# Optimization experiments

Hardware: AMD Instinct MI355X
Metric: run time of the kernel (lower is better)

## Reference

```python
import jax, jax.numpy as jnp
import numpy as np

N, B, C, IC = 4096, 4, 64, 32  # seq len, batch, in_channels, inter_channels
BN_EPS = 1e-5


def setup_inputs() -> dict:
    key = jax.random.key(0)
    ks = jax.random.split(key, 12)
    s = 0.05
    return {
        "x_thisBranch": jax.random.normal(ks[0], (N, B, C), jnp.float32),
        "x_otherBranch": jax.random.normal(ks[1], (N, B, C), jnp.float32),
        "g_w": jax.random.normal(ks[2], (IC, C), jnp.float32) * s,
        "g_b": jax.random.normal(ks[3], (IC,), jnp.float32) * s,
        "theta_w": jax.random.normal(ks[4], (IC, C), jnp.float32) * s,
        "theta_b": jax.random.normal(ks[5], (IC,), jnp.float32) * s,
        "phi_w": jax.random.normal(ks[6], (IC, C), jnp.float32) * s,
        "phi_b": jax.random.normal(ks[7], (IC,), jnp.float32) * s,
        "wz_w": jax.random.normal(ks[8], (C, IC), jnp.float32) * s,
        "wz_b": jax.random.normal(ks[9], (C,), jnp.float32) * s,
        "bn_gamma": jax.random.normal(ks[10], (C,), jnp.float32) * s + 1.0,
        "bn_beta": jax.random.normal(ks[11], (C,), jnp.float32) * s,
    }


def reference(x_thisBranch, x_otherBranch, g_w, g_b, theta_w, theta_b,
              phi_w, phi_b, wz_w, wz_b, bn_gamma, bn_beta):
    # [N,B,C] -> [B,C,N] as in torch permute(1,2,0)
    xt = jnp.transpose(x_thisBranch, (1, 2, 0))   # (B,C,N)
    xo = jnp.transpose(x_otherBranch, (1, 2, 0))  # (B,C,N)

    # 1x1 conv1d == per-position linear over channels
    g_x = jnp.einsum('ic,bcn->bni', g_w, xt) + g_b            # (B,N,IC)
    theta_x = jnp.einsum('ic,bcn->bin', theta_w, xt) + theta_b[:, None]  # (B,IC,N)
    phi_x = jnp.einsum('ic,bcn->bni', phi_w, xo) + phi_b      # (B,N,IC)

    # f = phi_x @ theta_x : rows indexed by other-branch positions
    f = jnp.einsum('bni,bim->bnm', phi_x, theta_x)            # (B,N,N)
    a = jax.nn.softmax(f, axis=-1)                            # embedded mode

    y = jnp.einsum('bnm,bmi->bni', a, g_x)                    # (B,N,IC)
    y = jnp.transpose(y, (0, 2, 1))                           # (B,IC,N)

    # W_z: 1x1 conv + BatchNorm1d (training-mode batch stats)
    wy = jnp.einsum('ci,bin->bcn', wz_w, y) + wz_b[:, None]   # (B,C,N)
    mean = wy.mean(axis=(0, 2), keepdims=True)
    var = wy.var(axis=(0, 2), keepdims=True)
    wy = (wy - mean) / jnp.sqrt(var + BN_EPS) * bn_gamma[:, None] + bn_beta[:, None]

    return wy + xt
```

## Files before the change

### kernel.cpp

```cpp
#include <hip/hip_runtime.h>
#include <hip/hip_bf16.h>
#include <math.h>

typedef unsigned short ushort_t;
typedef __attribute__((ext_vector_type(8))) short short8;
typedef __attribute__((ext_vector_type(4))) float float4v;

#define NN 4096
#define BB 4
#define CC 64
#define ICH 32

#define OFF_QB 0
#define OFF_KB 262144
#define OFF_VT 524288
#define OFF_OP 786432

static __device__ __forceinline__ ushort_t f2b(float f) {
  union { float f; unsigned u; } v;
  v.f = f;
  return (ushort_t)((v.u + 0x8000u) >> 16);
}
static __device__ __forceinline__ unsigned pack2(float x, float y) {
  return (unsigned)f2b(x) | ((unsigned)f2b(y) << 16);
}
static __device__ __forceinline__ short8 cvt8lds(const float* p) {
  short8 r;
#pragma unroll
  for (int j = 0; j < 8; j++) r[j] = (short)f2b(p[j]);
  return r;
}

__global__ __launch_bounds__(256) void proj_kernel(
    const float* __restrict__ xt, const float* __restrict__ xo,
    const float* __restrict__ gw, const float* __restrict__ gb,
    const float* __restrict__ tw, const float* __restrict__ tb,
    const float* __restrict__ pw, const float* __restrict__ pb,
    ushort_t* __restrict__ Qb, ushort_t* __restrict__ Kb,
    ushort_t* __restrict__ Vt) {
  __shared__ float xls[64 * 68];
  __shared__ float wls[ICH * 68];
  __shared__ float bls[ICH];
  __shared__ ushort_t ol[2304];

  int t = threadIdx.x;
  int wv = t >> 6, lane = t & 63, l15 = lane & 15, quad = lane >> 4;
  int b = blockIdx.y, z = blockIdx.z;
  int n0 = blockIdx.x * 64;

  const float* xsrc = (z == 1) ? xo : xt;
  const float* W = (z == 0) ? tw : (z == 1) ? pw : gw;
  const float* Bv = (z == 0) ? tb : (z == 1) ? pb : gb;

#pragma unroll
  for (int it = 0; it < 4; it++) {
    int lin = it * 256 + t;
    int row = lin >> 4, seg = lin & 15;
    float4 v = *(const float4*)(xsrc + ((size_t)(n0 + row) * BB + b) * CC + seg * 4);
    *(float4*)(xls + row * 68 + seg * 4) = v;
  }
#pragma unroll
  for (int it = 0; it < 2; it++) {
    int lin = it * 256 + t;
    int row = lin >> 4, seg = lin & 15;
    float4 v = *(const float4*)(W + (size_t)row * CC + seg * 4);
    *(float4*)(wls + row * 68 + seg * 4) = v;
  }
  if (t < ICH) bls[t] = Bv[t];
  __syncthreads();

  const float* xr = xls + (wv * 16 + l15) * 68;
  short8 a0 = cvt8lds(xr + quad * 8);
  short8 a1 = cvt8lds(xr + 32 + quad * 8);

#pragma unroll
  for (int h = 0; h < 2; h++) {
    int i = h * 16 + l15;
    short8 b0 = cvt8lds(wls + i * 68 + quad * 8);
    short8 b1 = cvt8lds(wls + i * 68 + 32 + quad * 8);
    float bias = bls[i];
    float4v acc = {bias, bias, bias, bias};
    acc = __builtin_amdgcn_mfma_f32_16x16x32_bf16(a0, b0, acc, 0, 0, 0);
    acc = __builtin_amdgcn_mfma_f32_16x16x32_bf16(a1, b1, acc, 0, 0, 0);
    if (z < 2) {
#pragma unroll
      for (int r = 0; r < 4; r++)
        ol[(wv * 16 + quad * 4 + r) * 36 + i] = f2b(acc[r]);
    } else {
#pragma unroll
      for (int r = 0; r < 4; r++)
        ol[i * 68 + wv * 16 + quad * 4 + r] = f2b(acc[r]);
    }
  }
  __syncthreads();

  if (z < 2) {
    ushort_t* dst = (z == 0) ? Kb : Qb;
    int row = t >> 2, seg = t & 3;
    short8 v;
#pragma unroll
    for (int k = 0; k < 8; k++) v[k] = (short)ol[row * 36 + seg * 8 + k];
    *(short8*)(dst + ((size_t)b * NN + n0 + row) * ICH + seg * 8) = v;
  } else {
    int i = t & 31, seg = t >> 5;
    short8 v;
#pragma unroll
    for (int k = 0; k < 8; k++) v[k] = (short)ol[i * 68 + seg * 8 + k];
    *(short8*)(Vt + (size_t)(b * ICH + i) * NN + n0 + seg * 8) = v;
  }
}

__global__ __launch_bounds__(256) void attn_kernel(
    const ushort_t* __restrict__ Qb, const ushort_t* __restrict__ Kb,
    const ushort_t* __restrict__ Vt, float* __restrict__ OP,
    float* __restrict__ LS, int splits) {
  int t = threadIdx.x;
  int wv = t >> 6, lane = t & 63, l15 = lane & 15, quad = lane >> 4;
  int s = blockIdx.y, b = blockIdx.z;
  int q0 = blockIdx.x * 256 + wv * 64;
  int kspan = NN / splits;

  short8 qf[4];
#pragma unroll
  for (int f = 0; f < 4; f++)
    qf[f] = *(const short8*)(Qb + ((size_t)b * NN + q0 + f * 16 + l15) * ICH +
                             quad * 8);

  float4v o[4][2];
#pragma unroll
  for (int f = 0; f < 4; f++) {
    o[f][0] = (float4v){0.f, 0.f, 0.f, 0.f};
    o[f][1] = (float4v){0.f, 0.f, 0.f, 0.f};
  }
  float lsp[4] = {0.f, 0.f, 0.f, 0.f};

  const ushort_t* Kbb = Kb + (size_t)b * NN * ICH;
  const ushort_t* Vtb = Vt + (size_t)b * ICH * NN;
  int mbeg = s * kspan, mend = mbeg + kspan;

  const bool lowq = (quad < 2);
  const bool evenq = ((quad & 1) == 0);

  for (int m0 = mbeg; m0 < mend; m0 += 32) {
    const ushort_t* kp = Kbb + (size_t)(m0 + l15) * ICH + quad * 8;
    short8 kf0 = *(const short8*)(kp);
    short8 kf1 = *(const short8*)(kp + 16 * ICH);
    const ushort_t* vp = Vtb + (size_t)l15 * NN + m0 + quad * 8;
    short8 vf0 = *(const short8*)(vp);
    short8 vf1 = *(const short8*)(vp + 16 * NN);

#pragma unroll
    for (int f = 0; f < 4; f++) {
      float4v z = {0.f, 0.f, 0.f, 0.f};
      float4v st0 = __builtin_amdgcn_mfma_f32_16x16x32_bf16(kf0, qf[f], z, 0, 0, 0);
      float4v st1 = __builtin_amdgcn_mfma_f32_16x16x32_bf16(kf1, qf[f], z, 0, 0, 0);

      float p0[4], p1[4];
#pragma unroll
      for (int r = 0; r < 4; r++) {
        p0[r] = __expf(fminf(st0[r], 60.f));
        p1[r] = __expf(fminf(st1[r], 60.f));
        lsp[f] += p0[r] + p1[r];
      }
      unsigned d0 = pack2(p0[0], p0[1]);
      unsigned d1 = pack2(p0[2], p0[3]);
      unsigned d2 = pack2(p1[0], p1[1]);
      unsigned d3 = pack2(p1[2], p1[3]);
      unsigned e0 = lowq ? d2 : d0, e1 = lowq ? d3 : d1;
      unsigned k0 = lowq ? d0 : d2, k1 = lowq ? d1 : d3;
      unsigned r0 = (unsigned)__shfl_xor((int)e0, 32, 64);
      unsigned r1 = (unsigned)__shfl_xor((int)e1, 32, 64);
      unsigned a0 = lowq ? k0 : r0;
      unsigned a1 = lowq ? k1 : r1;
      unsigned a2 = lowq ? r0 : k0;
      unsigned a3 = lowq ? r1 : k1;
      unsigned f0 = evenq ? a2 : a0, f1 = evenq ? a3 : a1;
      unsigned g0 = evenq ? a0 : a2, g1 = evenq ? a1 : a3;
      unsigned s0w = (unsigned)__shfl_xor((int)f0, 16, 64);
      unsigned s1w = (unsigned)__shfl_xor((int)f1, 16, 64);
      unsigned w0 = evenq ? g0 : s0w;
      unsigned w1 = evenq ? g1 : s1w;
      unsigned w2 = evenq ? s0w : g0;
      unsigned w3 = evenq ? s1w : g1;

      union { unsigned u[4]; short8 s8; } pu;
      pu.u[0] = w0; pu.u[1] = w1; pu.u[2] = w2; pu.u[3] = w3;
      short8 pf = pu.s8;

      o[f][0] = __builtin_amdgcn_mfma_f32_16x16x32_bf16(pf, vf0, o[f][0], 0, 0, 0);
      o[f][1] = __builtin_amdgcn_mfma_f32_16x16x32_bf16(pf, vf1, o[f][1], 0, 0, 0);
    }
  }

  size_t base = (size_t)(b * splits + s) * NN;
#pragma unroll
  for (int f = 0; f < 4; f++) {
    float v = lsp[f];
    v += __shfl_xor(v, 16, 64);
    v += __shfl_xor(v, 32, 64);
    if (quad == 0) LS[base + q0 + f * 16 + l15] = v;
#pragma unroll
    for (int r = 0; r < 4; r++) {
      int q = q0 + f * 16 + quad * 4 + r;
      float* op = OP + (base + q) * ICH;
      op[l15] = o[f][0][r];
      op[16 + l15] = o[f][1][r];
    }
  }
}

__global__ __launch_bounds__(256) void wz_kernel(
    const float* __restrict__ OP, const float* __restrict__ LS,
    const float* __restrict__ wz_w, const float* __restrict__ wz_b,
    float* __restrict__ WY, float* __restrict__ SP, int splits) {
  __shared__ float yl[64 * 36];
  __shared__ float lsum[64];
  __shared__ float red1[256], red2[256];

  int b = blockIdx.y, n0 = blockIdx.x * 64, t = threadIdx.x;
  int blkid = b * 64 + blockIdx.x;

  if (t < 64) {
    float ssum = 0.f;
    for (int sp = 0; sp < splits; sp++)
      ssum += LS[(size_t)(b * splits + sp) * NN + n0 + t];
    lsum[t] = ssum;
  }
  __syncthreads();
#pragma unroll
  for (int it = 0; it < 8; it++) {
    int lin = it * 256 + t;
    int i = lin & 31, dn = lin >> 5;
    float sacc = 0.f;
    for (int sp = 0; sp < splits; sp++)
      sacc += OP[((size_t)(b * splits + sp) * NN + n0 + dn) * ICH + i];
    yl[dn * 36 + i] = sacc / lsum[dn];
  }
  __syncthreads();

  int c = t >> 2, sub = t & 3;
  float4 w4[8];
#pragma unroll
  for (int j = 0; j < 8; j++) w4[j] = ((const float4*)(wz_w + c * ICH))[j];
  float bc = wz_b[c];
  float s1 = 0.f, s2 = 0.f;
#pragma unroll
  for (int d = 0; d < 16; d++) {
    int dn = sub * 16 + d;
    const float4* y4 = (const float4*)(yl + dn * 36);
    float acc = bc;
#pragma unroll
    for (int j = 0; j < 8; j++) {
      float4 y = y4[j];
      acc += w4[j].x * y.x + w4[j].y * y.y + w4[j].z * y.z + w4[j].w * y.w;
    }
    WY[((size_t)(b * CC + c)) * NN + n0 + dn] = acc;
    s1 += acc;
    s2 += acc * acc;
  }
  red1[t] = s1;
  red2[t] = s2;
  __syncthreads();
  if (t < 64) {
    float a1 = red1[t * 4] + red1[t * 4 + 1] + red1[t * 4 + 2] + red1[t * 4 + 3];
    float a2 = red2[t * 4] + red2[t * 4 + 1] + red2[t * 4 + 2] + red2[t * 4 + 3];
    SP[(size_t)blkid * 64 + t] = a1;
    SP[16384 + (size_t)blkid * 64 + t] = a2;
  }
}

__global__ __launch_bounds__(256) void stats_kernel(
    const float* __restrict__ SP, const float* __restrict__ gamma,
    const float* __restrict__ beta, float* __restrict__ AB) {
  __shared__ double r1[256], r2[256];
  int c = blockIdx.x, t = threadIdx.x;
  r1[t] = (double)SP[(size_t)t * 64 + c];
  r2[t] = (double)SP[16384 + (size_t)t * 64 + c];
  __syncthreads();
  for (int off = 128; off > 0; off >>= 1) {
    if (t < off) {
      r1[t] += r1[t + off];
      r2[t] += r2[t + off];
    }
    __syncthreads();
  }
  if (t == 0) {
    double inv = 1.0 / (double)(BB * NN);
    double mean = r1[0] * inv;
    double var = r2[0] * inv - mean * mean;
    if (var < 0.0) var = 0.0;
    double rstd = 1.0 / sqrt(var + 1e-5);
    float A = gamma[c] * (float)rstd;
    AB[c] = A;
    AB[64 + c] = beta[c] - (float)mean * A;
  }
}

__global__ __launch_bounds__(256) void norm_kernel(
    const float* __restrict__ WY, const float* __restrict__ AB,
    const float* __restrict__ xthis, float* __restrict__ out) {
  __shared__ float xl[64 * 65];
  __shared__ float abr[128];
  int b = blockIdx.y, n0 = blockIdx.x * 64, t = threadIdx.x;
  if (t < 128) abr[t] = AB[t];
#pragma unroll
  for (int it = 0; it < 16; it++) {
    int lin = it * 256 + t;
    int c = lin & 63, dn = lin >> 6;
    xl[dn * 65 + c] = xthis[((size_t)(n0 + dn) * BB + b) * CC + c];
  }
  __syncthreads();
#pragma unroll
  for (int it = 0; it < 16; it++) {
    int lin = it * 256 + t;
    int c = lin >> 6, dn = lin & 63;
    size_t idx = ((size_t)(b * CC + c)) * NN + n0 + dn;
    out[idx] = WY[idx] * abr[c] + abr[64 + c] + xl[dn * 65 + c];
  }
}

extern "C" void kernel_launch(void* const* d_in, const int* in_sizes, int n_in,
                              void* d_out, int out_size, void* d_ws,
                              size_t ws_size, hipStream_t stream) {
  const float* x_this = (const float*)d_in[0];
  const float* x_other = (const float*)d_in[1];
  const float* g_w = (const float*)d_in[2];
  const float* g_b = (const float*)d_in[3];
  const float* th_w = (const float*)d_in[4];
  const float* th_b = (const float*)d_in[5];
  const float* ph_w = (const float*)d_in[6];
  const float* ph_b = (const float*)d_in[7];
  const float* wz_w = (const float*)d_in[8];
  const float* wz_b = (const float*)d_in[9];
  const float* gamma = (const float*)d_in[10];
  const float* beta = (const float*)d_in[11];
  float* out = (float*)d_out;

  float* ws = (float*)d_ws;
  ushort_t* Qb = (ushort_t*)(ws + OFF_QB);
  ushort_t* Kb = (ushort_t*)(ws + OFF_KB);
  ushort_t* Vt = (ushort_t*)(ws + OFF_VT);

  int splits = 8;
  while (splits > 1 &&
         ws_size < (size_t)(786432 + (size_t)splits * 540672 + 32768 +
                            1048576 + 128) * 4)
    splits >>= 1;
  float* OP = ws + OFF_OP;
  float* LS = OP + (size_t)splits * 524288;
  float* SP = LS + (size_t)splits * 16384;
  float* WY = SP + 32768;
  float* AB = WY + 1048576;

  hipLaunchKernelGGL(proj_kernel, dim3(NN / 64, BB, 3), dim3(256), 0, stream,
                     x_this, x_other, g_w, g_b, th_w, th_b, ph_w, ph_b,
                     Qb, Kb, Vt);
  hipLaunchKernelGGL(attn_kernel, dim3(NN / 256, splits, BB), dim3(256), 0,
                     stream, Qb, Kb, Vt, OP, LS, splits);
  hipLaunchKernelGGL(wz_kernel, dim3(NN / 64, BB), dim3(256), 0, stream,
                     OP, LS, wz_w, wz_b, WY, SP, splits);
  hipLaunchKernelGGL(stats_kernel, dim3(CC), dim3(256), 0, stream,
                     SP, gamma, beta, AB);
  hipLaunchKernelGGL(norm_kernel, dim3(NN / 64, BB), dim3(256), 0, stream,
                     WY, AB, x_this, out);
}
```

Baseline: 145.7 us.

## Prefetch K/V tiles in attention, fuse BN stats into norm, raise splits

```diff
diff --git a/kernel.cpp b/kernel.cpp
--- a/kernel.cpp
+++ b/kernel.cpp
@@ -141,19 +141,29 @@
   const bool lowq = (quad < 2);
   const bool evenq = ((quad & 1) == 0);
 
+  const ushort_t* kp = Kbb + (size_t)(mbeg + l15) * ICH + quad * 8;
+  const ushort_t* vp = Vtb + (size_t)l15 * NN + mbeg + quad * 8;
+  short8 kc0 = *(const short8*)(kp);
+  short8 kc1 = *(const short8*)(kp + 16 * ICH);
+  short8 vc0 = *(const short8*)(vp);
+  short8 vc1 = *(const short8*)(vp + 16 * NN);
+
   for (int m0 = mbeg; m0 < mend; m0 += 32) {
-    const ushort_t* kp = Kbb + (size_t)(m0 + l15) * ICH + quad * 8;
-    short8 kf0 = *(const short8*)(kp);
-    short8 kf1 = *(const short8*)(kp + 16 * ICH);
-    const ushort_t* vp = Vtb + (size_t)l15 * NN + m0 + quad * 8;
-    short8 vf0 = *(const short8*)(vp);
-    short8 vf1 = *(const short8*)(vp + 16 * NN);
+    short8 kn0, kn1, vn0, vn1;
+    if (m0 + 32 < mend) {
+      const ushort_t* kpn = Kbb + (size_t)(m0 + 32 + l15) * ICH + quad * 8;
+      const ushort_t* vpn = Vtb + (size_t)l15 * NN + (m0 + 32) + quad * 8;
+      kn0 = *(const short8*)(kpn);
+      kn1 = *(const short8*)(kpn + 16 * ICH);
+      vn0 = *(const short8*)(vpn);
+      vn1 = *(const short8*)(vpn + 16 * NN);
+    }
 
 #pragma unroll
     for (int f = 0; f < 4; f++) {
       float4v z = {0.f, 0.f, 0.f, 0.f};
-      float4v st0 = __builtin_amdgcn_mfma_f32_16x16x32_bf16(kf0, qf[f], z, 0, 0, 0);
-      float4v st1 = __builtin_amdgcn_mfma_f32_16x16x32_bf16(kf1, qf[f], z, 0, 0, 0);
+      float4v st0 = __builtin_amdgcn_mfma_f32_16x16x32_bf16(kc0, qf[f], z, 0, 0, 0);
+      float4v st1 = __builtin_amdgcn_mfma_f32_16x16x32_bf16(kc1, qf[f], z, 0, 0, 0);
 
       float p0[4], p1[4];
 #pragma unroll
@@ -187,9 +197,10 @@
       pu.u[0] = w0; pu.u[1] = w1; pu.u[2] = w2; pu.u[3] = w3;
       short8 pf = pu.s8;
 
-      o[f][0] = __builtin_amdgcn_mfma_f32_16x16x32_bf16(pf, vf0, o[f][0], 0, 0, 0);
-      o[f][1] = __builtin_amdgcn_mfma_f32_16x16x32_bf16(pf, vf1, o[f][1], 0, 0, 0);
-    }
+      o[f][0] = __builtin_amdgcn_mfma_f32_16x16x32_bf16(pf, vc0, o[f][0], 0, 0, 0);
+      o[f][1] = __builtin_amdgcn_mfma_f32_16x16x32_bf16(pf, vc1, o[f][1], 0, 0, 0);
+    }
+    kc0 = kn0; kc1 = kn1; vc0 = vn0; vc1 = vn1;
   }
 
   size_t base = (size_t)(b * splits + s) * NN;
@@ -269,45 +280,43 @@
   }
 }
 
-__global__ __launch_bounds__(256) void stats_kernel(
+__global__ __launch_bounds__(256) void norm_kernel(
     const float* __restrict__ SP, const float* __restrict__ gamma,
-    const float* __restrict__ beta, float* __restrict__ AB) {
-  __shared__ double r1[256], r2[256];
-  int c = blockIdx.x, t = threadIdx.x;
-  r1[t] = (double)SP[(size_t)t * 64 + c];
-  r2[t] = (double)SP[16384 + (size_t)t * 64 + c];
-  __syncthreads();
-  for (int off = 128; off > 0; off >>= 1) {
-    if (t < off) {
-      r1[t] += r1[t + off];
-      r2[t] += r2[t + off];
-    }
-    __syncthreads();
-  }
-  if (t == 0) {
+    const float* __restrict__ beta, const float* __restrict__ WY,
+    const float* __restrict__ xthis, float* __restrict__ out) {
+  __shared__ double rd1[256], rd2[256];
+  __shared__ float abr[128];
+  __shared__ float xl[64 * 65];
+  int b = blockIdx.y, n0 = blockIdx.x * 64, t = threadIdx.x;
+
+  {
+    int cc = t & 63, part = t >> 6;
+    double d1 = 0.0, d2 = 0.0;
+    for (int k = part * 64; k < part * 64 + 64; k++) {
+      d1 += (double)SP[(size_t)k * 64 + cc];
+      d2 += (double)SP[16384 + (size_t)k * 64 + cc];
+    }
+    rd1[t] = d1;
+    rd2[t] = d2;
+  }
+#pragma unroll
+  for (int it = 0; it < 16; it++) {
+    int lin = it * 256 + t;
+    int c = lin & 63, dn = lin >> 6;
+    xl[dn * 65 + c] = xthis[((size_t)(n0 + dn) * BB + b) * CC + c];
+  }
+  __syncthreads();
+  if (t < 64) {
+    double a1 = rd1[t] + rd1[64 + t] + rd1[128 + t] + rd1[192 + t];
+    double a2 = rd2[t] + rd2[64 + t] + rd2[128 + t] + rd2[192 + t];
     double inv = 1.0 / (double)(BB * NN);
-    double mean = r1[0] * inv;
-    double var = r2[0] * inv - mean * mean;
+    double mean = a1 * inv;
+    double var = a2 * inv - mean * mean;
     if (var < 0.0) var = 0.0;
     double rstd = 1.0 / sqrt(var + 1e-5);
-    float A = gamma[c] * (float)rstd;
-    AB[c] = A;
-    AB[64 + c] = beta[c] - (float)mean * A;
-  }
-}
-
-__global__ __launch_bounds__(256) void norm_kernel(
-    const float* __restrict__ WY, const float* __restrict__ AB,
-    const float* __restrict__ xthis, float* __restrict__ out) {
-  __shared__ float xl[64 * 65];
-  __shared__ float abr[128];
-  int b = blockIdx.y, n0 = blockIdx.x * 64, t = threadIdx.x;
-  if (t < 128) abr[t] = AB[t];
-#pragma unroll
-  for (int it = 0; it < 16; it++) {
-    int lin = it * 256 + t;
-    int c = lin & 63, dn = lin >> 6;
-    xl[dn * 65 + c] = xthis[((size_t)(n0 + dn) * BB + b) * CC + c];
+    float A = gamma[t] * (float)rstd;
+    abr[t] = A;
+    abr[64 + t] = beta[t] - (float)mean * A;
   }
   __syncthreads();
 #pragma unroll
@@ -341,16 +350,15 @@
   ushort_t* Kb = (ushort_t*)(ws + OFF_KB);
   ushort_t* Vt = (ushort_t*)(ws + OFF_VT);
 
-  int splits = 8;
+  int splits = 16;
   while (splits > 1 &&
          ws_size < (size_t)(786432 + (size_t)splits * 540672 + 32768 +
-                            1048576 + 128) * 4)
+                            1048576) * 4)
     splits >>= 1;
   float* OP = ws + OFF_OP;
   float* LS = OP + (size_t)splits * 524288;
   float* SP = LS + (size_t)splits * 16384;
   float* WY = SP + 32768;
-  float* AB = WY + 1048576;
 
   hipLaunchKernelGGL(proj_kernel, dim3(NN / 64, BB, 3), dim3(256), 0, stream,
                      x_this, x_other, g_w, g_b, th_w, th_b, ph_w, ph_b,
@@ -359,8 +367,6 @@
                      stream, Qb, Kb, Vt, OP, LS, splits);
   hipLaunchKernelGGL(wz_kernel, dim3(NN / 64, BB), dim3(256), 0, stream,
                      OP, LS, wz_w, wz_b, WY, SP, splits);
-  hipLaunchKernelGGL(stats_kernel, dim3(CC), dim3(256), 0, stream,
-                     SP, gamma, beta, AB);
   hipLaunchKernelGGL(norm_kernel, dim3(NN / 64, BB), dim3(256), 0, stream,
-                     WY, AB, x_this, out);
-}
+                     SP, gamma, beta, WY, x_this, out);
+}
```

Measured after the change: 175.3 us. 20.3% more time.
